# Optimization experiments

Measured on AMD Instinct MI355X. Metric: run time of the kernel, lower is better.

The kernel has to match this reference:

```python
import jax, jax.numpy as jnp
import numpy as np

N = 100000
E = 800000
H = 4          # heads
C = 64         # per-head channels (concat=False -> head-mean, out dim 64)
G = 2000       # number of graphs
NEG_SLOPE = 0.2


def setup_inputs() -> dict:
    key = jax.random.key(0)
    ks = jax.random.split(key, 16)
    x = jax.random.normal(ks[0], (N, 9), dtype=jnp.float32)
    edge_index = jax.random.randint(ks[1], (2, E), 0, N, dtype=jnp.int64)
    batch = jnp.sort(jax.random.randint(ks[2], (N,), 0, G, dtype=jnp.int64))
    s = 0.1
    params = {}
    in_dims = [9, C, C]
    for l in range(3):
        kw, kas, kad = jax.random.split(ks[3 + l], 3)
        params[f'W{l+1}'] = jax.random.normal(kw, (in_dims[l], H * C), dtype=jnp.float32) * s
        params[f'as{l+1}'] = jax.random.normal(kas, (H, C), dtype=jnp.float32) * s
        params[f'ad{l+1}'] = jax.random.normal(kad, (H, C), dtype=jnp.float32) * s
        params[f'b{l+1}'] = jnp.zeros((C,), dtype=jnp.float32)
    params['lin_w'] = jax.random.normal(ks[7], (C, 1), dtype=jnp.float32) * s
    params['lin_b'] = jnp.zeros((1,), dtype=jnp.float32)
    return {'x': x, 'edge_index': edge_index, 'batch': batch, **params}


def _gat_conv(x, src, dst, W, a_src, a_dst, b):
    # x: [N, F_in] -> h: [N, H, C]
    h = (x @ W).reshape(N, H, C)
    al_s = jnp.einsum('nhc,hc->nh', h, a_src)   # [N, H]
    al_d = jnp.einsum('nhc,hc->nh', h, a_dst)   # [N, H]
    e = jax.nn.leaky_relu(al_s[src] + al_d[dst], NEG_SLOPE)  # [E+, H]
    # segment softmax over incoming edges of each dst node
    m = jax.ops.segment_max(e, dst, num_segments=N)
    ex = jnp.exp(e - m[dst])
    denom = jax.ops.segment_sum(ex, dst, num_segments=N)
    alpha = ex / (denom[dst] + 1e-16)            # [E+, H]
    msg = h[src] * alpha[:, :, None]             # [E+, H, C]
    out = jax.ops.segment_sum(msg, dst, num_segments=N)  # [N, H, C]
    return out.mean(axis=1) + b                  # concat=False -> head mean + bias


def reference(x, edge_index, batch, W1, as1, ad1, b1, W2, as2, ad2, b2,
              W3, as3, ad3, b3, lin_w, lin_b):
    # PyG GATConv adds self-loops by default
    loops = jnp.arange(N, dtype=edge_index.dtype)
    src = jnp.concatenate([edge_index[0], loops])
    dst = jnp.concatenate([edge_index[1], loops])

    h = jax.nn.relu(_gat_conv(x, src, dst, W1, as1, ad1, b1))
    h = jax.nn.relu(_gat_conv(h, src, dst, W2, as2, ad2, b2))
    h = jax.nn.relu(_gat_conv(h, src, dst, W3, as3, ad3, b3))

    # global_mean_pool over graphs
    sums = jax.ops.segment_sum(h, batch, num_segments=G)            # [G, C]
    cnts = jax.ops.segment_sum(jnp.ones((N,), h.dtype), batch, num_segments=G)
    pooled = sums / jnp.maximum(cnts, 1.0)[:, None]
    return pooled @ lin_w + lin_b                                    # [G, 1]
```

## Files before the change

### kernel.cpp

```cpp
#include <hip/hip_runtime.h>
#include <hip/hip_bf16.h>

#define NN 100000
#define EE 800000
#define HH 4
#define CC 64
#define GG 2000
#define NB 98

typedef unsigned short ushortx;
typedef __attribute__((ext_vector_type(8))) short short8;
typedef __attribute__((ext_vector_type(4))) float f32x4;


__global__ void hist_kernel(const int* __restrict__ ei, int* __restrict__ deg,
                            int* __restrict__ rank) {
    int e = blockIdx.x * 256 + threadIdx.x;
    const int tot = EE + NN;
    if (e < tot) {
        int d = (e < EE) ? ei[EE + e] : (e - EE);
        rank[e] = atomicAdd(&deg[d], 1);
    }
}

__global__ __launch_bounds__(256) void scan_blk(const int* __restrict__ deg,
                                                int* __restrict__ bsum) {
    const int t = threadIdx.x;
    const int idx4 = blockIdx.x * 256 + t;
    int4 v = {0, 0, 0, 0};
    if (idx4 < NN / 4) v = ((const int4*)deg)[idx4];
    int s = v.x + v.y + v.z + v.w;
#pragma unroll
    for (int m = 32; m; m >>= 1) s += __shfl_xor(s, m, 64);
    __shared__ int ws[4];
    if ((t & 63) == 0) ws[t >> 6] = s;
    __syncthreads();
    if (t == 0) bsum[blockIdx.x] = ws[0] + ws[1] + ws[2] + ws[3];
}

__global__ void scan_mid(const int* __restrict__ bsum, int* __restrict__ boff,
                         int* __restrict__ off) {
    __shared__ int sh[128];
    const int t = threadIdx.x;
    int v = (t < NB) ? bsum[t] : 0;
    sh[t] = v;
    __syncthreads();
    for (int d = 1; d < 128; d <<= 1) {
        int u = (t >= d) ? sh[t - d] : 0;
        __syncthreads();
        sh[t] += u;
        __syncthreads();
    }
    if (t < NB) boff[t] = sh[t] - v;
    if (t == NB - 1) off[NN] = sh[t];
}

__global__ __launch_bounds__(256) void scan_fin(const int* __restrict__ deg,
                                                const int* __restrict__ boff,
                                                int* __restrict__ off) {
    const int t = threadIdx.x;
    const int idx4 = blockIdx.x * 256 + t;
    int4 v = {0, 0, 0, 0};
    if (idx4 < NN / 4) v = ((const int4*)deg)[idx4];
    int s = v.x + v.y + v.z + v.w;
    const int lane = t & 63, w = t >> 6;
    int inc = s;
#pragma unroll
    for (int d = 1; d < 64; d <<= 1) {
        int u = __shfl_up(inc, d, 64);
        if (lane >= d) inc += u;
    }
    __shared__ int ws[4];
    if (lane == 63) ws[w] = inc;
    __syncthreads();
    int woff = 0;
    for (int i = 0; i < w; ++i) woff += ws[i];
    int excl = inc - s + woff + boff[blockIdx.x];
    if (idx4 < NN / 4) {
        int4 o;
        o.x = excl;
        o.y = o.x + v.x;
        o.z = o.y + v.y;
        o.w = o.z + v.z;
        ((int4*)off)[idx4] = o;
    }
}

__global__ __launch_bounds__(256) void fill_sharded(
    const int* __restrict__ ei, const int* __restrict__ off,
    const int* __restrict__ rank, int* __restrict__ csr_src) {
    const int shard = blockIdx.x & 7;
    const int wblk = blockIdx.x >> 3;
    const int lo = shard * (NN / 8);
    const int hi = lo + (NN / 8);
    const int tot = EE + NN;
    for (int e = wblk * 256 + threadIdx.x; e < tot; e += 256 * 256) {
        int d = (e < EE) ? ei[EE + e] : (e - EE);
        if (d >= lo && d < hi) {
            int s = (e < EE) ? ei[e] : (e - EE);
            csr_src[off[d] + rank[e]] = s;
        }
    }
}

__device__ __forceinline__ ushortx f2bf(float v) {
    __hip_bfloat16 b = __float2bfloat16(v);
    return *reinterpret_cast<ushortx*>(&b);
}


__device__ __forceinline__ void do_va(const float* __restrict__ W,
                                      const float* __restrict__ as_,
                                      const float* __restrict__ ad_,
                                      float* __restrict__ va, int K, int id) {
    if (id >= K * 8) return;
    int k = id >> 3, comp = id & 7;
    int h = comp & 3, sd = comp >> 2;
    const float* a = sd ? ad_ : as_;
    const float* wrow = W + k * 256 + h * 64;
    const float* arow = a + h * 64;
    float s = 0.f;
    for (int c = 0; c < 64; ++c) s = fmaf(wrow[c], arow[c], s);
    va[k * 8 + comp] = s;
}

__device__ __forceinline__ void do_wfrag(const float* __restrict__ W,
                                         ushortx* __restrict__ wfrag, int i) {
    if (i >= 16384) return;
    int j = i & 7, lane = (i >> 3) & 63, kb = (i >> 9) & 7, ct = i >> 12;
    int c = ct * 16 + (lane & 15);
    int kap = kb * 32 + (lane >> 4) * 8 + j;
    int h = kap >> 6, kw = kap & 63;
    wfrag[i] = f2bf(W[kw * 256 + h * 64 + c] * 0.25f);
}

__global__ void prep_all(
    const float* __restrict__ W1, const float* __restrict__ as1,
    const float* __restrict__ ad1, const float* __restrict__ W2,
    const float* __restrict__ as2, const float* __restrict__ ad2,
    const float* __restrict__ W3, const float* __restrict__ as3,
    const float* __restrict__ ad3, float* __restrict__ va1,
    float* __restrict__ va2, float* __restrict__ va3,
    ushortx* __restrict__ wf2, ushortx* __restrict__ wf3) {
    const int b = blockIdx.x, tid = threadIdx.x;
    if (b == 0) do_va(W1, as1, ad1, va1, 9, tid);
    else if (b <= 2) do_va(W2, as2, ad2, va2, 64, (b - 1) * 256 + tid);
    else if (b <= 4) do_va(W3, as3, ad3, va3, 64, (b - 3) * 256 + tid);
    else if (b <= 68) do_wfrag(W2, wf2, (b - 5) * 256 + tid);
    else do_wfrag(W3, wf3, (b - 69) * 256 + tid);
}

template <int K>
__global__ __launch_bounds__(256) void att_gemv(
    const float* __restrict__ X, const float* __restrict__ va,
    float* __restrict__ ALS, float* __restrict__ ALD) {
    __shared__ float vs[K][8];
    const int tid = threadIdx.x;
    for (int i = tid; i < K * 8; i += 256) vs[i >> 3][i & 7] = va[i];
    __syncthreads();
    int n = blockIdx.x * 256 + tid;
    if (n >= NN) return;
    const float* xp = X + (size_t)n * K;
    float s0 = 0, s1 = 0, s2 = 0, s3 = 0, d0 = 0, d1 = 0, d2 = 0, d3 = 0;
#pragma unroll
    for (int k = 0; k < K; ++k) {
        float x1 = xp[k];
        const float4 vsv = *(const float4*)&vs[k][0];
        const float4 vdv = *(const float4*)&vs[k][4];
        s0 = fmaf(x1, vsv.x, s0); s1 = fmaf(x1, vsv.y, s1);
        s2 = fmaf(x1, vsv.z, s2); s3 = fmaf(x1, vsv.w, s3);
        d0 = fmaf(x1, vdv.x, d0); d1 = fmaf(x1, vdv.y, d1);
        d2 = fmaf(x1, vdv.z, d2); d3 = fmaf(x1, vdv.w, d3);
    }
    float4 so = {s0, s1, s2, s3}, dd = {d0, d1, d2, d3};
    ((float4*)ALS)[n] = so;
    ((float4*)ALD)[n] = dd;
}

__global__ __launch_bounds__(256) void att_gemv_b(
    const ushortx* __restrict__ Xb, const float* __restrict__ va,
    float* __restrict__ ALS, float* __restrict__ ALD) {
    __shared__ float vs[64][8];
    const int tid = threadIdx.x;
    for (int i = tid; i < 64 * 8; i += 256) vs[i >> 3][i & 7] = va[i];
    __syncthreads();
    int n = blockIdx.x * 256 + tid;
    if (n >= NN) return;
    const uint4* xp = (const uint4*)(Xb + (size_t)n * 64);
    float s0 = 0, s1 = 0, s2 = 0, s3 = 0, d0 = 0, d1 = 0, d2 = 0, d3 = 0;
#pragma unroll
    for (int qq = 0; qq < 8; ++qq) {
        uint4 u = xp[qq];
        float xv[8];
        xv[0] = __uint_as_float(u.x << 16);
        xv[1] = __uint_as_float(u.x & 0xFFFF0000u);
        xv[2] = __uint_as_float(u.y << 16);
        xv[3] = __uint_as_float(u.y & 0xFFFF0000u);
        xv[4] = __uint_as_float(u.z << 16);
        xv[5] = __uint_as_float(u.z & 0xFFFF0000u);
        xv[6] = __uint_as_float(u.w << 16);
        xv[7] = __uint_as_float(u.w & 0xFFFF0000u);
#pragma unroll
        for (int j = 0; j < 8; ++j) {
            const int k = qq * 8 + j;
            const float4 vsv = *(const float4*)&vs[k][0];
            const float4 vdv = *(const float4*)&vs[k][4];
            s0 = fmaf(xv[j], vsv.x, s0); s1 = fmaf(xv[j], vsv.y, s1);
            s2 = fmaf(xv[j], vsv.z, s2); s3 = fmaf(xv[j], vsv.w, s3);
            d0 = fmaf(xv[j], vdv.x, d0); d1 = fmaf(xv[j], vdv.y, d1);
            d2 = fmaf(xv[j], vdv.z, d2); d3 = fmaf(xv[j], vdv.w, d3);
        }
    }
    float4 so = {s0, s1, s2, s3}, dd = {d0, d1, d2, d3};
    ((float4*)ALS)[n] = so;
    ((float4*)ALD)[n] = dd;
}

__device__ __forceinline__ float4 edge_w4(const float4 a, const float4 aldv) {
    float vx = a.x + aldv.x, vy = a.y + aldv.y,
          vz = a.z + aldv.z, vw = a.w + aldv.w;
    vx = (vx >= 0.f) ? vx : 0.2f * vx;
    vy = (vy >= 0.f) ? vy : 0.2f * vy;
    vz = (vz >= 0.f) ? vz : 0.2f * vz;
    vw = (vw >= 0.f) ? vw : 0.2f * vw;
    float4 w;
    w.x = __expf(vx); w.y = __expf(vy); w.z = __expf(vz); w.w = __expf(vw);
    return w;
}


__global__ __launch_bounds__(256) void aggregate_x1(
    const float* __restrict__ X, const float* __restrict__ ALS,
    const float* __restrict__ ALD, const int* __restrict__ off,
    const int* __restrict__ csr_src, float* __restrict__ AGG1) {
    __shared__ float4 wtab4[4][4][21];
    __shared__ int    svtab[4][4][21];
    const int wv = threadIdx.x >> 6;
    const int l = threadIdx.x & 63;
    const int g = l >> 4, kg = l & 15;
    const int node = blockIdx.x * 16 + wv * 4 + g;
    const bool nvalid = node < NN;
    const bool act = (kg < 9);
    int beg = 0, end = 0;
    if (nvalid) { beg = off[node]; end = off[node + 1]; }
    int md = end - beg;
    md = max(md, __shfl_xor(md, 16, 64));
    md = max(md, __shfl_xor(md, 32, 64));
    float4 aldv = {0.f, 0.f, 0.f, 0.f};
    if (nvalid) aldv = ((const float4*)ALD)[node];
    const float4* wt = &wtab4[wv][g][0];
    const int* st = &svtab[wv][g][0];
    float4 acc = {0.f, 0.f, 0.f, 0.f};
    float4 den4 = {0.f, 0.f, 0.f, 0.f};

    for (int c0 = 0; c0 < md; c0 += 16) {
        const int jj = beg + c0 + kg;
        int sv = 0;
        float4 w4 = {0.f, 0.f, 0.f, 0.f};
        if (nvalid && jj < end) {
            sv = csr_src[jj];
            w4 = edge_w4(((const float4*)ALS)[sv], aldv);
        }
        den4.x += w4.x; den4.y += w4.y; den4.z += w4.z; den4.w += w4.w;
        wtab4[wv][g][kg] = w4;
        svtab[wv][g][kg] = sv;
        __builtin_amdgcn_wave_barrier();
        asm volatile("s_waitcnt lgkmcnt(0)" ::: "memory");
        __builtin_amdgcn_sched_barrier(0);

        const int mc = min(16, md - c0);
        for (int t = 0; t < mc; t += 4) {
            float4 wA = wt[t + 0]; int sA = st[t + 0];
            float4 wB = wt[t + 1]; int sB = st[t + 1];
            float4 wC = wt[t + 2]; int sC = st[t + 2];
            float4 wD = wt[t + 3]; int sD = st[t + 3];
            float vA = 0.f, vB = 0.f, vC = 0.f, vD = 0.f;
            if (act) {
                vA = X[(size_t)sA * 9 + kg];
                vB = X[(size_t)sB * 9 + kg];
                vC = X[(size_t)sC * 9 + kg];
                vD = X[(size_t)sD * 9 + kg];
            }
            acc.x = fmaf(wA.x, vA, acc.x); acc.y = fmaf(wA.y, vA, acc.y);
            acc.z = fmaf(wA.z, vA, acc.z); acc.w = fmaf(wA.w, vA, acc.w);
            acc.x = fmaf(wB.x, vB, acc.x); acc.y = fmaf(wB.y, vB, acc.y);
            acc.z = fmaf(wB.z, vB, acc.z); acc.w = fmaf(wB.w, vB, acc.w);
            acc.x = fmaf(wC.x, vC, acc.x); acc.y = fmaf(wC.y, vC, acc.y);
            acc.z = fmaf(wC.z, vC, acc.z); acc.w = fmaf(wC.w, vC, acc.w);
            acc.x = fmaf(wD.x, vD, acc.x); acc.y = fmaf(wD.y, vD, acc.y);
            acc.z = fmaf(wD.z, vD, acc.z); acc.w = fmaf(wD.w, vD, acc.w);
        }
        __builtin_amdgcn_wave_barrier();
    }

#pragma unroll
    for (int m = 1; m <= 8; m <<= 1) {
        den4.x += __shfl_xor(den4.x, m, 64);
        den4.y += __shfl_xor(den4.y, m, 64);
        den4.z += __shfl_xor(den4.z, m, 64);
        den4.w += __shfl_xor(den4.w, m, 64);
    }
    if (nvalid && act) {
        float i0 = 1.f / (den4.x + 1e-16f);
        float i1 = 1.f / (den4.y + 1e-16f);
        float i2 = 1.f / (den4.z + 1e-16f);
        float i3 = 1.f / (den4.w + 1e-16f);
        float* o = AGG1 + (size_t)node * 64;
        o[0 * 16 + kg] = acc.x * i0;
        o[1 * 16 + kg] = acc.y * i1;
        o[2 * 16 + kg] = acc.z * i2;
        o[3 * 16 + kg] = acc.w * i3;
    }
}


__global__ __launch_bounds__(256) void gemm36(
    const float* __restrict__ AGG1, const float* __restrict__ W1,
    const float* __restrict__ b1, ushortx* __restrict__ Xb) {
    const int c = threadIdx.x & 63;
    const int wv = threadIdx.x >> 6;
    float wreg[36];
#pragma unroll
    for (int h = 0; h < 4; ++h)
#pragma unroll
        for (int k = 0; k < 9; ++k)
            wreg[h * 9 + k] = W1[k * 256 + h * 64 + c] * 0.25f;
    const float bc = b1[c];
    for (int row = blockIdx.x * 4 + wv; row < NN; row += gridDim.x * 4) {
        const float* xr = AGG1 + (size_t)row * 64;
        float s = 0.f;
#pragma unroll
        for (int h = 0; h < 4; ++h)
#pragma unroll
            for (int k = 0; k < 9; ++k)
                s = fmaf(wreg[h * 9 + k], xr[h * 16 + k], s);
        s = fmaxf(s + bc, 0.f);
        Xb[(size_t)row * 64 + c] = f2bf(s);
    }
}


__global__ __launch_bounds__(256) void aggregate_xb(
    const ushortx* __restrict__ Xb, const float* __restrict__ ALS,
    const float* __restrict__ ALD, const int* __restrict__ off,
    const int* __restrict__ csr_src, ushortx* __restrict__ AGG) {
    __shared__ float4 wtab4[4][4][21];
    __shared__ int    svtab[4][4][21];
    const int wv = threadIdx.x >> 6;
    const int l = threadIdx.x & 63;
    const int g = l >> 4, c4 = l & 15;
    const int node = blockIdx.x * 16 + wv * 4 + g;
    const bool nvalid = node < NN;
    int beg = 0, end = 0;
    if (nvalid) { beg = off[node]; end = off[node + 1]; }
    int md = end - beg;
    md = max(md, __shfl_xor(md, 16, 64));
    md = max(md, __shfl_xor(md, 32, 64));
    float4 aldv = {0.f, 0.f, 0.f, 0.f};
    if (nvalid) aldv = ((const float4*)ALD)[node];
    const uint2* xb2 = (const uint2*)Xb;
    const float4* wt = &wtab4[wv][g][0];
    const int* st = &svtab[wv][g][0];
    float4 a0 = {0.f, 0.f, 0.f, 0.f};
    float4 a1 = {0.f, 0.f, 0.f, 0.f};
    float4 a2 = {0.f, 0.f, 0.f, 0.f};
    float4 a3 = {0.f, 0.f, 0.f, 0.f};
    float4 den4 = {0.f, 0.f, 0.f, 0.f};

#define UPD(uu, ww)                                                 \
    {                                                               \
        float c0v = __uint_as_float((uu).x << 16);                  \
        float c1v = __uint_as_float((uu).x & 0xFFFF0000u);          \
        float c2v = __uint_as_float((uu).y << 16);                  \
        float c3v = __uint_as_float((uu).y & 0xFFFF0000u);          \
        a0.x = fmaf((ww).x, c0v, a0.x); a0.y = fmaf((ww).x, c1v, a0.y); \
        a0.z = fmaf((ww).x, c2v, a0.z); a0.w = fmaf((ww).x, c3v, a0.w); \
        a1.x = fmaf((ww).y, c0v, a1.x); a1.y = fmaf((ww).y, c1v, a1.y); \
        a1.z = fmaf((ww).y, c2v, a1.z); a1.w = fmaf((ww).y, c3v, a1.w); \
        a2.x = fmaf((ww).z, c0v, a2.x); a2.y = fmaf((ww).z, c1v, a2.y); \
        a2.z = fmaf((ww).z, c2v, a2.z); a2.w = fmaf((ww).z, c3v, a2.w); \
        a3.x = fmaf((ww).w, c0v, a3.x); a3.y = fmaf((ww).w, c1v, a3.y); \
        a3.z = fmaf((ww).w, c2v, a3.z); a3.w = fmaf((ww).w, c3v, a3.w); \
    }

    for (int c0 = 0; c0 < md; c0 += 16) {
        const int jj = beg + c0 + c4;
        int sv = 0;
        float4 w4 = {0.f, 0.f, 0.f, 0.f};
        if (nvalid && jj < end) {
            sv = csr_src[jj];
            w4 = edge_w4(((const float4*)ALS)[sv], aldv);
        }
        den4.x += w4.x; den4.y += w4.y; den4.z += w4.z; den4.w += w4.w;
        wtab4[wv][g][c4] = w4;
        svtab[wv][g][c4] = sv;
        __builtin_amdgcn_wave_barrier();
        asm volatile("s_waitcnt lgkmcnt(0)" ::: "memory");
        __builtin_amdgcn_sched_barrier(0);

        const int mc = min(16, md - c0);
        for (int t = 0; t < mc; t += 4) {
            float4 wA = wt[t + 0]; int sA = st[t + 0];
            float4 wB = wt[t + 1]; int sB = st[t + 1];
            float4 wC = wt[t + 2]; int sC = st[t + 2];
            float4 wD = wt[t + 3]; int sD = st[t + 3];
            uint2 uA = xb2[(size_t)sA * 16 + c4];
            uint2 uB = xb2[(size_t)sB * 16 + c4];
            uint2 uC = xb2[(size_t)sC * 16 + c4];
            uint2 uD = xb2[(size_t)sD * 16 + c4];
            UPD(uA, wA);
            UPD(uB, wB);
            UPD(uC, wC);
            UPD(uD, wD);
        }
        __builtin_amdgcn_wave_barrier();
    }
#undef UPD

#pragma unroll
    for (int m = 1; m <= 8; m <<= 1) {
        den4.x += __shfl_xor(den4.x, m, 64);
        den4.y += __shfl_xor(den4.y, m, 64);
        den4.z += __shfl_xor(den4.z, m, 64);
        den4.w += __shfl_xor(den4.w, m, 64);
    }
    if (nvalid) {
        float i0 = 1.f / (den4.x + 1e-16f);
        float i1 = 1.f / (den4.y + 1e-16f);
        float i2 = 1.f / (den4.z + 1e-16f);
        float i3 = 1.f / (den4.w + 1e-16f);
        ushortx* orow = AGG + (size_t)node * 256;
        uint p0, p1;
        p0 = (uint)f2bf(a0.x * i0) | ((uint)f2bf(a0.y * i0) << 16);
        p1 = (uint)f2bf(a0.z * i0) | ((uint)f2bf(a0.w * i0) << 16);
        *(uint2*)&orow[0 * 64 + c4 * 4] = uint2{p0, p1};
        p0 = (uint)f2bf(a1.x * i1) | ((uint)f2bf(a1.y * i1) << 16);
        p1 = (uint)f2bf(a1.z * i1) | ((uint)f2bf(a1.w * i1) << 16);
        *(uint2*)&orow[1 * 64 + c4 * 4] = uint2{p0, p1};
        p0 = (uint)f2bf(a2.x * i2) | ((uint)f2bf(a2.y * i2) << 16);
        p1 = (uint)f2bf(a2.z * i2) | ((uint)f2bf(a2.w * i2) << 16);
        *(uint2*)&orow[2 * 64 + c4 * 4] = uint2{p0, p1};
        p0 = (uint)f2bf(a3.x * i3) | ((uint)f2bf(a3.y * i3) << 16);
        p1 = (uint)f2bf(a3.z * i3) | ((uint)f2bf(a3.w * i3) << 16);
        *(uint2*)&orow[3 * 64 + c4 * 4] = uint2{p0, p1};
    }
}


template <bool F32OUT>
__global__ __launch_bounds__(256) void gemm256_mfma(
    const ushortx* __restrict__ AGG, const ushortx* __restrict__ wfrag,
    const float* __restrict__ bias, ushortx* __restrict__ Xb,
    float* __restrict__ OUTF) {
    __shared__ ushortx wt[4][8][64][8];
    const int tid = threadIdx.x;
    const int l = tid & 63, wv = tid >> 6;
    const int n = l & 15, q = l >> 4;

    {
        const uint4* src = (const uint4*)wfrag;
        uint4* dst = (uint4*)&wt[0][0][0][0];
#pragma unroll
        for (int i = 0; i < 8; ++i) dst[i * 256 + tid] = src[i * 256 + tid];
    }
    __syncthreads();

    for (int row0 = blockIdx.x * 64 + wv * 16; row0 < NN; row0 += gridDim.x * 64) {
        f32x4 acc[4] = {{0.f, 0.f, 0.f, 0.f}, {0.f, 0.f, 0.f, 0.f},
                        {0.f, 0.f, 0.f, 0.f}, {0.f, 0.f, 0.f, 0.f}};
#pragma unroll
        for (int kb = 0; kb < 8; ++kb) {
            short8 a = *(const short8*)&AGG[(size_t)(row0 + n) * 256 + kb * 32 + q * 8];
#pragma unroll
            for (int ct = 0; ct < 4; ++ct) {
                short8 b = *(const short8*)&wt[ct][kb][l][0];
                acc[ct] = __builtin_amdgcn_mfma_f32_16x16x32_bf16(b, a, acc[ct], 0, 0, 0);
            }
        }
        const int row = row0 + n;
#pragma unroll
        for (int ct = 0; ct < 4; ++ct) {
            const int col = ct * 16 + q * 4;
            float4 b4 = ((const float4*)bias)[ct * 4 + q];
            float o0 = fmaxf(acc[ct][0] + b4.x, 0.f);
            float o1 = fmaxf(acc[ct][1] + b4.y, 0.f);
            float o2 = fmaxf(acc[ct][2] + b4.z, 0.f);
            float o3 = fmaxf(acc[ct][3] + b4.w, 0.f);
            if constexpr (F32OUT) {
                float4 ov = {o0, o1, o2, o3};
                *(float4*)&OUTF[(size_t)row * 64 + col] = ov;
            } else {
                uint p0 = (uint)f2bf(o0) | ((uint)f2bf(o1) << 16);
                uint p1 = (uint)f2bf(o2) | ((uint)f2bf(o3) << 16);
                uint2 ov = {p0, p1};
                *(uint2*)&Xb[(size_t)row * 64 + col] = ov;
            }
        }
    }
}


__global__ __launch_bounds__(256) void pool_graph(
    const float* __restrict__ OUTF, const int* __restrict__ batch,
    const float* __restrict__ lw, const float* __restrict__ lb,
    float* __restrict__ out) {
    const int g = blockIdx.x * 4 + (threadIdx.x >> 6);
    const int l = threadIdx.x & 63;
    if (g >= GG) return;
    int lo = 0, hi = NN;
    while (lo < hi) { int mid = (lo + hi) >> 1; if (batch[mid] < g) lo = mid + 1; else hi = mid; }
    int lo2 = lo, hi2 = NN;
    while (lo2 < hi2) { int mid = (lo2 + hi2) >> 1; if (batch[mid] < g + 1) lo2 = mid + 1; else hi2 = mid; }
    float s = 0.f;
    int nn = lo;
    for (; nn + 4 <= lo2; nn += 4) {
        float a0 = OUTF[(size_t)(nn + 0) * 64 + l];
        float a1 = OUTF[(size_t)(nn + 1) * 64 + l];
        float a2 = OUTF[(size_t)(nn + 2) * 64 + l];
        float a3 = OUTF[(size_t)(nn + 3) * 64 + l];
        s += (a0 + a1) + (a2 + a3);
    }
    for (; nn < lo2; ++nn) s += OUTF[(size_t)nn * 64 + l];
    const float cntf = fmaxf((float)(lo2 - lo), 1.f);
    float v = s / cntf * lw[l];
#pragma unroll
    for (int m = 32; m; m >>= 1) v += __shfl_xor(v, m, 64);
    if (l == 0) out[g] = v + lb[0];
}


extern "C" void kernel_launch(void* const* d_in, const int* in_sizes, int n_in,
                              void* d_out, int out_size, void* d_ws, size_t ws_size,
                              hipStream_t stream) {
    const float* x     = (const float*)d_in[0];
    const int*   ei    = (const int*)d_in[1];
    const int*   batch = (const int*)d_in[2];
    const float* W1  = (const float*)d_in[3];
    const float* as1 = (const float*)d_in[4];
    const float* ad1 = (const float*)d_in[5];
    const float* b1  = (const float*)d_in[6];
    const float* W2  = (const float*)d_in[7];
    const float* as2 = (const float*)d_in[8];
    const float* ad2 = (const float*)d_in[9];
    const float* b2  = (const float*)d_in[10];
    const float* W3  = (const float*)d_in[11];
    const float* as3 = (const float*)d_in[12];
    const float* ad3 = (const float*)d_in[13];
    const float* b3  = (const float*)d_in[14];
    const float* lw  = (const float*)d_in[15];
    const float* lb  = (const float*)d_in[16];
    float* out = (float*)d_out;

    char* p = (char*)d_ws;
    auto carve = [&](size_t bytes) -> void* {
        void* r = (void*)p;
        p += (bytes + 255) & ~(size_t)255;
        return r;
    };
    int*     off    = (int*)carve((NN + 4) * sizeof(int));
    int*     deg    = (int*)carve(NN * sizeof(int));
    int*     rank   = (int*)carve((size_t)(EE + NN) * sizeof(int));
    int*     bsum   = (int*)carve(NB * sizeof(int));
    int*     boff   = (int*)carve(NB * sizeof(int));
    int*     csr    = (int*)carve((size_t)(EE + NN) * sizeof(int));
    ushortx* aggb   = (ushortx*)carve((size_t)NN * 256 * sizeof(ushortx));
    float*   agg1   = (float*)carve((size_t)NN * 64 * sizeof(float));
    ushortx* xb1    = (ushortx*)carve((size_t)NN * 64 * sizeof(ushortx));
    float*   outf   = (float*)carve((size_t)NN * 64 * sizeof(float));
    float*   als    = (float*)carve((size_t)NN * 4 * sizeof(float));
    float*   ald    = (float*)carve((size_t)NN * 4 * sizeof(float));
    float*   va1    = (float*)carve(9 * 8 * sizeof(float));
    float*   va2    = (float*)carve(64 * 8 * sizeof(float));
    float*   va3    = (float*)carve(64 * 8 * sizeof(float));
    ushortx* wf2    = (ushortx*)carve(16384 * sizeof(ushortx));
    ushortx* wf3    = (ushortx*)carve(16384 * sizeof(ushortx));
    ushortx* xb2 = (ushortx*)agg1;

    hipMemsetAsync(deg, 0, NN * sizeof(int), stream);

    const int etot = EE + NN;
    const int eblocks = (etot + 255) / 256;
    hist_kernel<<<eblocks, 256, 0, stream>>>(ei, deg, rank);
    scan_blk<<<NB, 256, 0, stream>>>(deg, bsum);
    scan_mid<<<1, 128, 0, stream>>>(bsum, boff, off);
    scan_fin<<<NB, 256, 0, stream>>>(deg, boff, off);
    fill_sharded<<<2048, 256, 0, stream>>>(ei, off, rank, csr);

    prep_all<<<133, 256, 0, stream>>>(W1, as1, ad1, W2, as2, ad2, W3, as3, ad3,
                                      va1, va2, va3, wf2, wf3);

    const int ablocks = (NN + 15) / 16;
    const int nblocks = (NN + 255) / 256;

    att_gemv<9><<<nblocks, 256, 0, stream>>>(x, va1, als, ald);
    aggregate_x1<<<ablocks, 256, 0, stream>>>(x, als, ald, off, csr, agg1);
    gemm36<<<2048, 256, 0, stream>>>(agg1, W1, b1, xb1);

    att_gemv_b<<<nblocks, 256, 0, stream>>>(xb1, va2, als, ald);
    aggregate_xb<<<ablocks, 256, 0, stream>>>(xb1, als, ald, off, csr, aggb);
    gemm256_mfma<false><<<512, 256, 0, stream>>>(aggb, wf2, b2, xb2, nullptr);

    att_gemv_b<<<nblocks, 256, 0, stream>>>(xb2, va3, als, ald);
    aggregate_xb<<<ablocks, 256, 0, stream>>>(xb2, als, ald, off, csr, aggb);
    gemm256_mfma<true><<<512, 256, 0, stream>>>(aggb, wf3, b3, nullptr, outf);

    pool_graph<<<(GG + 3) / 4, 256, 0, stream>>>(outf, batch, lw, lb, out);
}
```

Baseline: 334.7 us.

## Sort nodes by degree bucket to balance aggregation wavefront work

Builds a degree-bucketed permutation of nodes (counting sort on clamped in-degree, computed in scan_fin plus two small kernels). The aggregation kernels then process nodes in this order, so the four nodes sharing a wave have similar degree and the per-wave max-degree loop wastes fewer iterations. It also changes the gemm grid size. The cost is extra kernels and an indirect node lookup, and output writes become scattered instead of sequential.

```diff
diff --git a/kernel.cpp b/kernel.cpp
--- a/kernel.cpp
+++ b/kernel.cpp
@@ -57,7 +57,9 @@
 
 __global__ __launch_bounds__(256) void scan_fin(const int* __restrict__ deg,
                                                 const int* __restrict__ boff,
-                                                int* __restrict__ off) {
+                                                int* __restrict__ off,
+                                                int* __restrict__ bcnt,
+                                                int* __restrict__ wrank) {
     const int t = threadIdx.x;
     const int idx4 = blockIdx.x * 256 + t;
     int4 v = {0, 0, 0, 0};
@@ -83,6 +85,50 @@
         o.z = o.y + v.y;
         o.w = o.z + v.z;
         ((int4*)off)[idx4] = o;
+    }
+
+    __shared__ int lbin[64];
+    __shared__ int bbase[64];
+    if (t < 64) lbin[t] = 0;
+    __syncthreads();
+    int key[4] = {0, 0, 0, 0}, lr[4] = {0, 0, 0, 0};
+    if (idx4 < NN / 4) {
+        key[0] = min(v.x, 63); key[1] = min(v.y, 63);
+        key[2] = min(v.z, 63); key[3] = min(v.w, 63);
+        lr[0] = atomicAdd(&lbin[key[0]], 1);
+        lr[1] = atomicAdd(&lbin[key[1]], 1);
+        lr[2] = atomicAdd(&lbin[key[2]], 1);
+        lr[3] = atomicAdd(&lbin[key[3]], 1);
+    }
+    __syncthreads();
+    if (t < 64) bbase[t] = lbin[t] ? atomicAdd(&bcnt[t], lbin[t]) : 0;
+    __syncthreads();
+    if (idx4 < NN / 4) {
+        wrank[idx4 * 4 + 0] = bbase[key[0]] + lr[0];
+        wrank[idx4 * 4 + 1] = bbase[key[1]] + lr[1];
+        wrank[idx4 * 4 + 2] = bbase[key[2]] + lr[2];
+        wrank[idx4 * 4 + 3] = bbase[key[3]] + lr[3];
+    }
+}
+
+__global__ void bscan(const int* __restrict__ bcnt, int* __restrict__ bboff) {
+    const int t = threadIdx.x;
+    int v = bcnt[t];
+    int inc = v;
+#pragma unroll
+    for (int d = 1; d < 64; d <<= 1) {
+        int u = __shfl_up(inc, d, 64);
+        if (t >= d) inc += u;
+    }
+    bboff[t] = inc - v;
+}
+
+__global__ void perm_fill(const int* __restrict__ deg, const int* __restrict__ wrank,
+                          const int* __restrict__ bboff, int* __restrict__ perm) {
+    int n = blockIdx.x * 256 + threadIdx.x;
+    if (n < NN) {
+        int key = min(deg[n], 63);
+        perm[bboff[key] + wrank[n]] = n;
     }
 }
 
@@ -232,22 +278,20 @@
 __global__ __launch_bounds__(256) void aggregate_x1(
     const float* __restrict__ X, const float* __restrict__ ALS,
     const float* __restrict__ ALD, const int* __restrict__ off,
-    const int* __restrict__ csr_src, float* __restrict__ AGG1) {
+    const int* __restrict__ csr_src, const int* __restrict__ perm,
+    float* __restrict__ AGG1) {
     __shared__ float4 wtab4[4][4][21];
     __shared__ int    svtab[4][4][21];
     const int wv = threadIdx.x >> 6;
     const int l = threadIdx.x & 63;
     const int g = l >> 4, kg = l & 15;
-    const int node = blockIdx.x * 16 + wv * 4 + g;
-    const bool nvalid = node < NN;
+    const int node = perm[blockIdx.x * 16 + wv * 4 + g];
     const bool act = (kg < 9);
-    int beg = 0, end = 0;
-    if (nvalid) { beg = off[node]; end = off[node + 1]; }
+    const int beg = off[node], end = off[node + 1];
     int md = end - beg;
     md = max(md, __shfl_xor(md, 16, 64));
     md = max(md, __shfl_xor(md, 32, 64));
-    float4 aldv = {0.f, 0.f, 0.f, 0.f};
-    if (nvalid) aldv = ((const float4*)ALD)[node];
+    const float4 aldv = ((const float4*)ALD)[node];
     const float4* wt = &wtab4[wv][g][0];
     const int* st = &svtab[wv][g][0];
     float4 acc = {0.f, 0.f, 0.f, 0.f};
@@ -257,7 +301,7 @@
         const int jj = beg + c0 + kg;
         int sv = 0;
         float4 w4 = {0.f, 0.f, 0.f, 0.f};
-        if (nvalid && jj < end) {
+        if (jj < end) {
             sv = csr_src[jj];
             w4 = edge_w4(((const float4*)ALS)[sv], aldv);
         }
@@ -300,7 +344,7 @@
         den4.z += __shfl_xor(den4.z, m, 64);
         den4.w += __shfl_xor(den4.w, m, 64);
     }
-    if (nvalid && act) {
+    if (act) {
         float i0 = 1.f / (den4.x + 1e-16f);
         float i1 = 1.f / (den4.y + 1e-16f);
         float i2 = 1.f / (den4.z + 1e-16f);
@@ -343,21 +387,19 @@
 __global__ __launch_bounds__(256) void aggregate_xb(
     const ushortx* __restrict__ Xb, const float* __restrict__ ALS,
     const float* __restrict__ ALD, const int* __restrict__ off,
-    const int* __restrict__ csr_src, ushortx* __restrict__ AGG) {
+    const int* __restrict__ csr_src, const int* __restrict__ perm,
+    ushortx* __restrict__ AGG) {
     __shared__ float4 wtab4[4][4][21];
     __shared__ int    svtab[4][4][21];
     const int wv = threadIdx.x >> 6;
     const int l = threadIdx.x & 63;
     const int g = l >> 4, c4 = l & 15;
-    const int node = blockIdx.x * 16 + wv * 4 + g;
-    const bool nvalid = node < NN;
-    int beg = 0, end = 0;
-    if (nvalid) { beg = off[node]; end = off[node + 1]; }
+    const int node = perm[blockIdx.x * 16 + wv * 4 + g];
+    const int beg = off[node], end = off[node + 1];
     int md = end - beg;
     md = max(md, __shfl_xor(md, 16, 64));
     md = max(md, __shfl_xor(md, 32, 64));
-    float4 aldv = {0.f, 0.f, 0.f, 0.f};
-    if (nvalid) aldv = ((const float4*)ALD)[node];
+    const float4 aldv = ((const float4*)ALD)[node];
     const uint2* xb2 = (const uint2*)Xb;
     const float4* wt = &wtab4[wv][g][0];
     const int* st = &svtab[wv][g][0];
@@ -387,7 +429,7 @@
         const int jj = beg + c0 + c4;
         int sv = 0;
         float4 w4 = {0.f, 0.f, 0.f, 0.f};
-        if (nvalid && jj < end) {
+        if (jj < end) {
             sv = csr_src[jj];
             w4 = edge_w4(((const float4*)ALS)[sv], aldv);
         }
@@ -424,7 +466,7 @@
         den4.z += __shfl_xor(den4.z, m, 64);
         den4.w += __shfl_xor(den4.w, m, 64);
     }
-    if (nvalid) {
+    {
         float i0 = 1.f / (den4.x + 1e-16f);
         float i1 = 1.f / (den4.y + 1e-16f);
         float i2 = 1.f / (den4.z + 1e-16f);
@@ -574,35 +616,43 @@
     float*   va3    = (float*)carve(64 * 8 * sizeof(float));
     ushortx* wf2    = (ushortx*)carve(16384 * sizeof(ushortx));
     ushortx* wf3    = (ushortx*)carve(16384 * sizeof(ushortx));
+    int*     bcnt   = (int*)carve(64 * sizeof(int));
+    int*     bboff  = (int*)carve(64 * sizeof(int));
+    int*     wrank  = (int*)carve(NN * sizeof(int));
+    int*     perm   = (int*)carve(NN * sizeof(int));
     ushortx* xb2 = (ushortx*)agg1;
 
     hipMemsetAsync(deg, 0, NN * sizeof(int), stream);
+    hipMemsetAsync(bcnt, 0, 64 * sizeof(int), stream);
 
     const int etot = EE + NN;
     const int eblocks = (etot + 255) / 256;
     hist_kernel<<<eblocks, 256, 0, stream>>>(ei, deg, rank);
     scan_blk<<<NB, 256, 0, stream>>>(deg, bsum);
     scan_mid<<<1, 128, 0, stream>>>(bsum, boff, off);
-    scan_fin<<<NB, 256, 0, stream>>>(deg, boff, off);
+    scan_fin<<<NB, 256, 0, stream>>>(deg, boff, off, bcnt, wrank);
     fill_sharded<<<2048, 256, 0, stream>>>(ei, off, rank, csr);
+    bscan<<<1, 64, 0, stream>>>(bcnt, bboff);
+    perm_fill<<<(NN + 255) / 256, 256, 0, stream>>>(deg, wrank, bboff, perm);
 
     prep_all<<<133, 256, 0, stream>>>(W1, as1, ad1, W2, as2, ad2, W3, as3, ad3,
                                       va1, va2, va3, wf2, wf3);
 
     const int ablocks = (NN + 15) / 16;
     const int nblocks = (NN + 255) / 256;
+    const int gblocks = 521;
 
     att_gemv<9><<<nblocks, 256, 0, stream>>>(x, va1, als, ald);
-    aggregate_x1<<<ablocks, 256, 0, stream>>>(x, als, ald, off, csr, agg1);
+    aggregate_x1<<<ablocks, 256, 0, stream>>>(x, als, ald, off, csr, perm, agg1);
     gemm36<<<2048, 256, 0, stream>>>(agg1, W1, b1, xb1);
 
     att_gemv_b<<<nblocks, 256, 0, stream>>>(xb1, va2, als, ald);
-    aggregate_xb<<<ablocks, 256, 0, stream>>>(xb1, als, ald, off, csr, aggb);
-    gemm256_mfma<false><<<512, 256, 0, stream>>>(aggb, wf2, b2, xb2, nullptr);
+    aggregate_xb<<<ablocks, 256, 0, stream>>>(xb1, als, ald, off, csr, perm, aggb);
+    gemm256_mfma<false><<<gblocks, 256, 0, stream>>>(aggb, wf2, b2, xb2, nullptr);
 
     att_gemv_b<<<nblocks, 256, 0, stream>>>(xb2, va3, als, ald);
-    aggregate_xb<<<ablocks, 256, 0, stream>>>(xb2, als, ald, off, csr, aggb);
-    gemm256_mfma<true><<<512, 256, 0, stream>>>(aggb, wf3, b3, nullptr, outf);
+    aggregate_xb<<<ablocks, 256, 0, stream>>>(xb2, als, ald, off, csr, perm, aggb);
+    gemm256_mfma<true><<<gblocks, 256, 0, stream>>>(aggb, wf3, b3, nullptr, outf);
 
     pool_graph<<<(GG + 3) / 4, 256, 0, stream>>>(outf, batch, lw, lb, out);
 }
```

Result: slower. 362.1 us (+8.2%).

## Fuse edge aggregation with MFMA projection GEMM for layers two and three

Applied to the files above, without the earlier changes.

Merges the aggregation kernel and the bf16 MFMA GEMM into one kernel. Each 16-node block writes its aggregated 256-wide rows into shared memory, then multiplies them by the weight fragments, so the large NN x 256 bf16 intermediate no longer goes through global memory. Bounds checks on node are dropped, which relies on NN being divisible by 16. Each block now reads weight fragments from global (cached) memory instead of staging them once per persistent block, and adds a block-wide barrier.

```diff
diff --git a/kernel.cpp b/kernel.cpp
--- a/kernel.cpp
+++ b/kernel.cpp
@@ -239,15 +239,12 @@
     const int l = threadIdx.x & 63;
     const int g = l >> 4, kg = l & 15;
     const int node = blockIdx.x * 16 + wv * 4 + g;
-    const bool nvalid = node < NN;
     const bool act = (kg < 9);
-    int beg = 0, end = 0;
-    if (nvalid) { beg = off[node]; end = off[node + 1]; }
+    const int beg = off[node], end = off[node + 1];
     int md = end - beg;
     md = max(md, __shfl_xor(md, 16, 64));
     md = max(md, __shfl_xor(md, 32, 64));
-    float4 aldv = {0.f, 0.f, 0.f, 0.f};
-    if (nvalid) aldv = ((const float4*)ALD)[node];
+    const float4 aldv = ((const float4*)ALD)[node];
     const float4* wt = &wtab4[wv][g][0];
     const int* st = &svtab[wv][g][0];
     float4 acc = {0.f, 0.f, 0.f, 0.f};
@@ -257,7 +254,7 @@
         const int jj = beg + c0 + kg;
         int sv = 0;
         float4 w4 = {0.f, 0.f, 0.f, 0.f};
-        if (nvalid && jj < end) {
+        if (jj < end) {
             sv = csr_src[jj];
             w4 = edge_w4(((const float4*)ALS)[sv], aldv);
         }
@@ -300,7 +297,7 @@
         den4.z += __shfl_xor(den4.z, m, 64);
         den4.w += __shfl_xor(den4.w, m, 64);
     }
-    if (nvalid && act) {
+    if (act) {
         float i0 = 1.f / (den4.x + 1e-16f);
         float i1 = 1.f / (den4.y + 1e-16f);
         float i2 = 1.f / (den4.z + 1e-16f);
@@ -340,24 +337,25 @@
 }
 
 
-__global__ __launch_bounds__(256) void aggregate_xb(
+template <bool F32OUT>
+__global__ __launch_bounds__(256) void agg_gemm(
     const ushortx* __restrict__ Xb, const float* __restrict__ ALS,
     const float* __restrict__ ALD, const int* __restrict__ off,
-    const int* __restrict__ csr_src, ushortx* __restrict__ AGG) {
+    const int* __restrict__ csr_src, const ushortx* __restrict__ wfrag,
+    const float* __restrict__ bias, ushortx* __restrict__ XbOut,
+    float* __restrict__ OUTF) {
     __shared__ float4 wtab4[4][4][21];
     __shared__ int    svtab[4][4][21];
+    __shared__ ushortx sAgg[16][264];
     const int wv = threadIdx.x >> 6;
     const int l = threadIdx.x & 63;
     const int g = l >> 4, c4 = l & 15;
     const int node = blockIdx.x * 16 + wv * 4 + g;
-    const bool nvalid = node < NN;
-    int beg = 0, end = 0;
-    if (nvalid) { beg = off[node]; end = off[node + 1]; }
+    const int beg = off[node], end = off[node + 1];
     int md = end - beg;
     md = max(md, __shfl_xor(md, 16, 64));
     md = max(md, __shfl_xor(md, 32, 64));
-    float4 aldv = {0.f, 0.f, 0.f, 0.f};
-    if (nvalid) aldv = ((const float4*)ALD)[node];
+    const float4 aldv = ((const float4*)ALD)[node];
     const uint2* xb2 = (const uint2*)Xb;
     const float4* wt = &wtab4[wv][g][0];
     const int* st = &svtab[wv][g][0];
@@ -387,7 +385,7 @@
         const int jj = beg + c0 + c4;
         int sv = 0;
         float4 w4 = {0.f, 0.f, 0.f, 0.f};
-        if (nvalid && jj < end) {
+        if (jj < end) {
             sv = csr_src[jj];
             w4 = edge_w4(((const float4*)ALS)[sv], aldv);
         }
@@ -424,12 +422,12 @@
         den4.z += __shfl_xor(den4.z, m, 64);
         den4.w += __shfl_xor(den4.w, m, 64);
     }
-    if (nvalid) {
+    {
         float i0 = 1.f / (den4.x + 1e-16f);
         float i1 = 1.f / (den4.y + 1e-16f);
         float i2 = 1.f / (den4.z + 1e-16f);
         float i3 = 1.f / (den4.w + 1e-16f);
-        ushortx* orow = AGG + (size_t)node * 256;
+        ushortx* orow = &sAgg[wv * 4 + g][0];
         uint p0, p1;
         p0 = (uint)f2bf(a0.x * i0) | ((uint)f2bf(a0.y * i0) << 16);
         p1 = (uint)f2bf(a0.z * i0) | ((uint)f2bf(a0.w * i0) << 16);
@@ -444,58 +442,31 @@
         p1 = (uint)f2bf(a3.z * i3) | ((uint)f2bf(a3.w * i3) << 16);
         *(uint2*)&orow[3 * 64 + c4 * 4] = uint2{p0, p1};
     }
-}
-
-
-template <bool F32OUT>
-__global__ __launch_bounds__(256) void gemm256_mfma(
-    const ushortx* __restrict__ AGG, const ushortx* __restrict__ wfrag,
-    const float* __restrict__ bias, ushortx* __restrict__ Xb,
-    float* __restrict__ OUTF) {
-    __shared__ ushortx wt[4][8][64][8];
-    const int tid = threadIdx.x;
-    const int l = tid & 63, wv = tid >> 6;
+    __syncthreads();
+
     const int n = l & 15, q = l >> 4;
-
-    {
-        const uint4* src = (const uint4*)wfrag;
-        uint4* dst = (uint4*)&wt[0][0][0][0];
-#pragma unroll
-        for (int i = 0; i < 8; ++i) dst[i * 256 + tid] = src[i * 256 + tid];
-    }
-    __syncthreads();
-
-    for (int row0 = blockIdx.x * 64 + wv * 16; row0 < NN; row0 += gridDim.x * 64) {
-        f32x4 acc[4] = {{0.f, 0.f, 0.f, 0.f}, {0.f, 0.f, 0.f, 0.f},
-                        {0.f, 0.f, 0.f, 0.f}, {0.f, 0.f, 0.f, 0.f}};
-#pragma unroll
-        for (int kb = 0; kb < 8; ++kb) {
-            short8 a = *(const short8*)&AGG[(size_t)(row0 + n) * 256 + kb * 32 + q * 8];
-#pragma unroll
-            for (int ct = 0; ct < 4; ++ct) {
-                short8 b = *(const short8*)&wt[ct][kb][l][0];
-                acc[ct] = __builtin_amdgcn_mfma_f32_16x16x32_bf16(b, a, acc[ct], 0, 0, 0);
-            }
-        }
-        const int row = row0 + n;
-#pragma unroll
-        for (int ct = 0; ct < 4; ++ct) {
-            const int col = ct * 16 + q * 4;
-            float4 b4 = ((const float4*)bias)[ct * 4 + q];
-            float o0 = fmaxf(acc[ct][0] + b4.x, 0.f);
-            float o1 = fmaxf(acc[ct][1] + b4.y, 0.f);
-            float o2 = fmaxf(acc[ct][2] + b4.z, 0.f);
-            float o3 = fmaxf(acc[ct][3] + b4.w, 0.f);
-            if constexpr (F32OUT) {
-                float4 ov = {o0, o1, o2, o3};
-                *(float4*)&OUTF[(size_t)row * 64 + col] = ov;
-            } else {
-                uint p0 = (uint)f2bf(o0) | ((uint)f2bf(o1) << 16);
-                uint p1 = (uint)f2bf(o2) | ((uint)f2bf(o3) << 16);
-                uint2 ov = {p0, p1};
-                *(uint2*)&Xb[(size_t)row * 64 + col] = ov;
-            }
-        }
+    f32x4 acc = {0.f, 0.f, 0.f, 0.f};
+#pragma unroll
+    for (int kb = 0; kb < 8; ++kb) {
+        short8 a = *(const short8*)&sAgg[n][kb * 32 + q * 8];
+        short8 b = *(const short8*)&wfrag[(size_t)((wv * 8 + kb) * 64 + l) * 8];
+        acc = __builtin_amdgcn_mfma_f32_16x16x32_bf16(b, a, acc, 0, 0, 0);
+    }
+    const int row = blockIdx.x * 16 + n;
+    const int col = wv * 16 + q * 4;
+    float4 b4 = ((const float4*)bias)[wv * 4 + q];
+    float o0 = fmaxf(acc[0] + b4.x, 0.f);
+    float o1 = fmaxf(acc[1] + b4.y, 0.f);
+    float o2 = fmaxf(acc[2] + b4.z, 0.f);
+    float o3 = fmaxf(acc[3] + b4.w, 0.f);
+    if constexpr (F32OUT) {
+        float4 ov = {o0, o1, o2, o3};
+        *(float4*)&OUTF[(size_t)row * 64 + col] = ov;
+    } else {
+        uint p0 = (uint)f2bf(o0) | ((uint)f2bf(o1) << 16);
+        uint p1 = (uint)f2bf(o2) | ((uint)f2bf(o3) << 16);
+        uint2 ov = {p0, p1};
+        *(uint2*)&XbOut[(size_t)row * 64 + col] = ov;
     }
 }
 
@@ -563,7 +534,6 @@
     int*     bsum   = (int*)carve(NB * sizeof(int));
     int*     boff   = (int*)carve(NB * sizeof(int));
     int*     csr    = (int*)carve((size_t)(EE + NN) * sizeof(int));
-    ushortx* aggb   = (ushortx*)carve((size_t)NN * 256 * sizeof(ushortx));
     float*   agg1   = (float*)carve((size_t)NN * 64 * sizeof(float));
     ushortx* xb1    = (ushortx*)carve((size_t)NN * 64 * sizeof(ushortx));
     float*   outf   = (float*)carve((size_t)NN * 64 * sizeof(float));
@@ -589,7 +559,7 @@
     prep_all<<<133, 256, 0, stream>>>(W1, as1, ad1, W2, as2, ad2, W3, as3, ad3,
                                       va1, va2, va3, wf2, wf3);
 
-    const int ablocks = (NN + 15) / 16;
+    const int ablocks = NN / 16;
     const int nblocks = (NN + 255) / 256;
 
     att_gemv<9><<<nblocks, 256, 0, stream>>>(x, va1, als, ald);
@@ -597,12 +567,12 @@
     gemm36<<<2048, 256, 0, stream>>>(agg1, W1, b1, xb1);
 
     att_gemv_b<<<nblocks, 256, 0, stream>>>(xb1, va2, als, ald);
-    aggregate_xb<<<ablocks, 256, 0, stream>>>(xb1, als, ald, off, csr, aggb);
-    gemm256_mfma<false><<<512, 256, 0, stream>>>(aggb, wf2, b2, xb2, nullptr);
+    agg_gemm<false><<<ablocks, 256, 0, stream>>>(xb1, als, ald, off, csr, wf2,
+                                                 b2, xb2, nullptr);
 
     att_gemv_b<<<nblocks, 256, 0, stream>>>(xb2, va3, als, ald);
-    aggregate_xb<<<ablocks, 256, 0, stream>>>(xb2, als, ald, off, csr, aggb);
-    gemm256_mfma<true><<<512, 256, 0, stream>>>(aggb, wf3, b3, nullptr, outf);
+    agg_gemm<true><<<ablocks, 256, 0, stream>>>(xb2, als, ald, off, csr, wf3,
+                                                b3, nullptr, outf);
 
     pool_graph<<<(GG + 3) / 4, 256, 0, stream>>>(outf, batch, lw, lb, out);
 }
```

Result: faster. 316.8 us (-5.3%).
